# Performance work log

Measured on AMD Instinct MI355X. Metric: run time of the kernel, lower is better.

Reference implementation:

```python
import jax, jax.numpy as jnp
import numpy as np

N = 100_000   # nodes per type
E = 800_000   # edges per relation
H = 128       # hidden_channels
O = 64        # out_channels
TIME_SCALE = 1.0
LN_EPS = 1e-5


def setup_inputs() -> dict:
    key = jax.random.key(0)
    ks = jax.random.split(key, 24)
    nrm = lambda k, shp, s=1.0: jax.random.normal(k, shp, jnp.float32) * s
    inp = {}
    inp["x_A"] = nrm(ks[0], (N, H))
    inp["x_B"] = nrm(ks[1], (N, H))
    inp["x_C"] = nrm(ks[2], (N, H))
    inp["t_A"] = jax.random.uniform(ks[3], (N,), jnp.float32) * 1000.0
    inp["t_B"] = jax.random.uniform(ks[4], (N,), jnp.float32) * 1000.0
    inp["t_C"] = jax.random.uniform(ks[5], (N,), jnp.float32) * 1000.0
    inp["edge1"] = jnp.stack([jax.random.randint(ks[6], (E,), 0, N),
                              jax.random.randint(ks[7], (E,), 0, N)]).astype(jnp.int32)
    inp["edge2"] = jnp.stack([jax.random.randint(ks[8], (E,), 0, N),
                              jax.random.randint(ks[9], (E,), 0, N)]).astype(jnp.int32)
    kk = 10
    for i in range(2):
        inp[f"Wl{i}"] = nrm(ks[kk], (H, H), 0.05); kk += 1
        inp[f"bl{i}"] = jnp.zeros((H,), jnp.float32)
        inp[f"W0{i}"] = nrm(ks[kk], (H, H), 0.05); kk += 1
        inp[f"b0{i}"] = jnp.zeros((H,), jnp.float32)
        inp[f"W1{i}"] = nrm(ks[kk], (H, H), 0.05); kk += 1
        inp[f"b1{i}"] = jnp.zeros((H,), jnp.float32)
        inp[f"gate{i}"] = jnp.asarray(0.5, jnp.float32)
        inp[f"lam{i}"] = jnp.asarray(0.1, jnp.float32)  # raw lambda
        inp[f"lng{i}"] = jnp.ones((H,), jnp.float32)
        inp[f"lnb{i}"] = jnp.zeros((H,), jnp.float32)
    inp["Wout"] = nrm(ks[kk], (H, O), 0.05)
    inp["bout"] = jnp.zeros((O,), jnp.float32)
    return inp


def _layer(h_src, h_dst, x0_dst, edge, t_src, t_dst,
           Wl, bl, W0, b0, W1, b1, gate, raw_lam, lng, lnb):
    s, d = edge[0], edge[1]
    n_dst = h_dst.shape[0]
    # per-edge time-decay weight
    lam = jax.nn.softplus(raw_lam) + 1e-8
    delta = jnp.maximum((t_dst[d] - t_src[s]) / TIME_SCALE, 0.0)
    w = jnp.exp(jnp.maximum(-lam * delta, -60.0))          # [E]
    # gather + weight + scatter-add  (propagate with aggr='add')
    msg = h_src[s] * w[:, None]                            # [E,H]
    agg = jax.ops.segment_sum(msg, d, num_segments=n_dst)  # [n_dst,H]
    deg = jnp.maximum(jax.ops.segment_sum(w, d, num_segments=n_dst), 1e-6)
    out = agg / deg[:, None]
    g = jax.nn.sigmoid(gate)
    y = out @ Wl + bl + (1.0 - g) * (h_dst @ W0 + b0) + g * (x0_dst @ W1 + b1)
    y = jax.nn.relu(y)
    mu = jnp.mean(y, axis=-1, keepdims=True)
    var = jnp.mean((y - mu) ** 2, axis=-1, keepdims=True)
    y = (y - mu) * jax.lax.rsqrt(var + LN_EPS) * lng + lnb
    # index_copy_: only nodes that appear as a destination get updated
    cnt = jax.ops.segment_sum(jnp.ones_like(w), d, num_segments=n_dst)
    return jnp.where((cnt > 0)[:, None], y, h_dst)


def reference(x_A, x_B, x_C, t_A, t_B, t_C, edge1, edge2,
              Wl0, bl0, W00, b00, W10, b10, gate0, lam0, lng0, lnb0,
              Wl1, bl1, W01, b01, W11, b11, gate1, lam1, lng1, lnb1,
              Wout, bout):
    # reversed(metapath): process (B,r2,C) with conv_idx=1 first, then (A,r1,B) with conv_idx=0
    h_C = _layer(x_B, x_C, x_C, edge2, t_B, t_C,
                 Wl1, bl1, W01, b01, W11, b11, gate1, lam1, lng1, lnb1)
    h_B = _layer(x_A, x_B, x_B, edge1, t_A, t_B,
                 Wl0, bl0, W00, b00, W10, b10, gate0, lam0, lng0, lnb0)
    del h_B  # target type is metapath[-1][2] == 'C'; B's update does not feed C
    return h_C @ Wout + bout
```

## Files before the change

### kernel.cpp

```cpp
#include <hip/hip_runtime.h>


#define HD 128
#define OD 64
#define SCAN_E 1024

typedef unsigned short u16;
typedef short v8s __attribute__((ext_vector_type(8)));
typedef float v4f __attribute__((ext_vector_type(4)));

union Frag {
    unsigned int u[4];
    uint4 q;
    v8s v;
};

__device__ __forceinline__ float softplus_f(float x) {
    return fmaxf(x, 0.0f) + log1pf(expf(-fabsf(x)));
}
__device__ __forceinline__ float sigmoid_f(float x) {
    return 1.0f / (1.0f + expf(-x));
}
__device__ __forceinline__ int swz(int r, int c) {
    int g = (c >> 2) ^ (r & 7);
    return r * 128 + g * 4 + (c & 3);
}

__device__ __forceinline__ void split_store(float x, u16* ph, u16* pl) {
    unsigned int b = __float_as_uint(x);
    unsigned int h = b & 0xffff0000u;
    *ph = (u16)(h >> 16);
    float r = x - __uint_as_float(h);
    *pl = (u16)(__float_as_uint(r) >> 16);
}

__device__ __forceinline__ void cvt_split8(const float* f, unsigned int* hi,
                                           unsigned int* lo) {
#pragma unroll
    for (int j = 0; j < 4; ++j) {
        unsigned int b0 = __float_as_uint(f[2 * j]);
        unsigned int b1 = __float_as_uint(f[2 * j + 1]);
        unsigned int h0 = b0 & 0xffff0000u;
        unsigned int h1 = b1 & 0xffff0000u;
        hi[j] = (h0 >> 16) | h1;
        float r0 = f[2 * j]     - __uint_as_float(h0);
        float r1 = f[2 * j + 1] - __uint_as_float(h1);
        lo[j] = (__float_as_uint(r0) >> 16) | (__float_as_uint(r1) & 0xffff0000u);
    }
}

__global__ __launch_bounds__(256) void k_hist(
    const int* __restrict__ edge, int* __restrict__ cnt, int E)
{
    int e = blockIdx.x * 256 + threadIdx.x;
    if (e < E) atomicAdd(cnt + edge[E + e], 1);
}

__global__ __launch_bounds__(256) void k_scan1(
    const int* __restrict__ cnt, int* __restrict__ offs,
    int* __restrict__ part, int N)
{
    __shared__ int sh[256];
    const int t = threadIdx.x;
    const int base = blockIdx.x * SCAN_E + t * 4;
    int v[4], sum = 0;
#pragma unroll
    for (int i = 0; i < 4; ++i) {
        int idx = base + i;
        v[i] = (idx < N) ? cnt[idx] : 0;
        sum += v[i];
    }
    sh[t] = sum;
    __syncthreads();
    for (int off = 1; off < 256; off <<= 1) {
        int x = (t >= off) ? sh[t - off] : 0;
        __syncthreads();
        sh[t] += x;
        __syncthreads();
    }
    int run = (t > 0) ? sh[t - 1] : 0;
    if (t == 255) part[blockIdx.x] = sh[t];
#pragma unroll
    for (int i = 0; i < 4; ++i) {
        int idx = base + i;
        if (idx < N) offs[idx] = run;
        run += v[i];
    }
}

__global__ __launch_bounds__(128) void k_scan2(int* __restrict__ part, int NB)
{
    __shared__ int sh[128];
    const int t = threadIdx.x;
    sh[t] = (t < NB) ? part[t] : 0;
    __syncthreads();
    for (int off = 1; off < 128; off <<= 1) {
        int x = (t >= off) ? sh[t - off] : 0;
        __syncthreads();
        sh[t] += x;
        __syncthreads();
    }
    if (t < NB) part[t] = (t > 0) ? sh[t - 1] : 0;
}

__global__ __launch_bounds__(256) void k_fillw(
    const int* __restrict__ edge, const float* __restrict__ tB,
    const float* __restrict__ tC, const float* __restrict__ lam_raw,
    const int* __restrict__ offs, const int* __restrict__ part,
    int* __restrict__ fillc, int2* __restrict__ srcw, int E)
{
    int e = blockIdx.x * 256 + threadIdx.x;
    if (e >= E) return;
    int s = edge[e];
    int d = edge[E + e];
    float lam = softplus_f(lam_raw[0]) + 1e-8f;
    float dt  = fmaxf(tC[d] - tB[s], 0.0f);
    float w   = expf(fmaxf(-lam * dt, -60.0f));
    int pos = offs[d] + part[d >> 10] + atomicAdd(fillc + d, 1);
    srcw[pos] = make_int2(s, __float_as_int(w));
}

__global__ __launch_bounds__(256) void k_wprep(
    const float* __restrict__ Wl, const float* __restrict__ W0,
    const float* __restrict__ W1, const float* __restrict__ Wout,
    const float* __restrict__ bl, const float* __restrict__ b0,
    const float* __restrict__ b1, const float* __restrict__ gatep,
    u16* __restrict__ wlh, u16* __restrict__ wll,
    u16* __restrict__ wch, u16* __restrict__ wcl,
    u16* __restrict__ woh, u16* __restrict__ wol, float* __restrict__ bc)
{
    int i = blockIdx.x * 256 + threadIdx.x;
    const float g = sigmoid_f(gatep[0]);
    if (i < 16384) {
        int n = i >> 7, k = i & 127;
        float a  = Wl[k * 128 + n];
        float w0 = W0[k * 128 + n];
        float w1 = W1[k * 128 + n];
        float c  = (1.f - g) * w0 + g * w1;
        int off = ((k >> 5) * 128 + n) * 32 + (k & 31);
        split_store(a, wlh + off, wll + off);
        split_store(c, wch + off, wcl + off);
    } else if (i < 24576) {
        int j = i - 16384;
        int n = j >> 7, k = j & 127;
        float v = Wout[k * 64 + n];
        int off = ((k >> 5) * 64 + n) * 32 + (k & 31);
        split_store(v, woh + off, wol + off);
    } else if (i < 24704) {
        int t = i - 24576;
        bc[t] = bl[t] + (1.f - g) * b0[t] + g * b1[t];
    }
}

__global__ __launch_bounds__(256) void k_gather(
    const float* __restrict__ xB, const int2* __restrict__ srcw,
    const int* __restrict__ offs, const int* __restrict__ part,
    const int* __restrict__ cnt, float* __restrict__ aggn, int N)
{
    const int wave = (blockIdx.x * 256 + threadIdx.x) >> 6;
    const int lane = threadIdx.x & 63;
    const int slot = lane >> 4;
    const int l4   = lane & 15;
    if (wave >= N) return;
    const int r    = wave;
    const int degc = cnt[r];

    float* dstp = aggn + (size_t)r * HD;
    if (degc == 0) {
        if (slot == 0) {
            *reinterpret_cast<float4*>(dstp + l4 * 4) = make_float4(0, 0, 0, 0);
            *reinterpret_cast<float4*>(dstp + 64 + l4 * 4) = make_float4(0, 0, 0, 0);
        }
        return;
    }

    const int start = offs[r] + part[r >> 10];
    float4 a0 = make_float4(0, 0, 0, 0), a1 = make_float4(0, 0, 0, 0);
    float sw = 0.f;
#pragma unroll 2
    for (int j = slot; j < degc; j += 4) {
        int2 swp = srcw[start + j];
        float w = __int_as_float(swp.y);
        const float* row = xB + (size_t)swp.x * HD;
        float4 x0 = *reinterpret_cast<const float4*>(row + l4 * 4);
        float4 x1 = *reinterpret_cast<const float4*>(row + 64 + l4 * 4);
        a0.x = fmaf(w, x0.x, a0.x); a0.y = fmaf(w, x0.y, a0.y);
        a0.z = fmaf(w, x0.z, a0.z); a0.w = fmaf(w, x0.w, a0.w);
        a1.x = fmaf(w, x1.x, a1.x); a1.y = fmaf(w, x1.y, a1.y);
        a1.z = fmaf(w, x1.z, a1.z); a1.w = fmaf(w, x1.w, a1.w);
        sw += w;
    }
#pragma unroll
    for (int m = 16; m <= 32; m <<= 1) {
        a0.x += __shfl_xor(a0.x, m); a0.y += __shfl_xor(a0.y, m);
        a0.z += __shfl_xor(a0.z, m); a0.w += __shfl_xor(a0.w, m);
        a1.x += __shfl_xor(a1.x, m); a1.y += __shfl_xor(a1.y, m);
        a1.z += __shfl_xor(a1.z, m); a1.w += __shfl_xor(a1.w, m);
        sw   += __shfl_xor(sw, m);
    }
    float inv = 1.0f / fmaxf(sw, 1e-6f);
    if (slot == 0) {
        a0.x *= inv; a0.y *= inv; a0.z *= inv; a0.w *= inv;
        a1.x *= inv; a1.y *= inv; a1.z *= inv; a1.w *= inv;
        *reinterpret_cast<float4*>(dstp + l4 * 4) = a0;
        *reinterpret_cast<float4*>(dstp + 64 + l4 * 4) = a1;
    }
}

__global__ __launch_bounds__(256) void k_fused(
    const float* __restrict__ xC, const float* __restrict__ aggn,
    const int* __restrict__ cnt,
    const u16* __restrict__ wlh, const u16* __restrict__ wll,
    const u16* __restrict__ wch, const u16* __restrict__ wcl,
    const u16* __restrict__ woh, const u16* __restrict__ wol,
    const float* __restrict__ bc, const float* __restrict__ lng,
    const float* __restrict__ lnb, const float* __restrict__ bout,
    float* __restrict__ out, int N)
{
    __shared__ float lds[4 * 16 * 128];

    const int lane = threadIdx.x & 63;
    const int wid  = threadIdx.x >> 6;
    const int lr   = lane & 15;
    const int kb   = lane >> 4;
    const int row0 = blockIdx.x * 128 + wid * 32;
    float* myl = lds + wid * 16 * 128;

    v4f acc[2][8] = {};

#pragma unroll
    for (int mat = 0; mat < 2; ++mat) {
        const float* Asrc = mat ? xC : aggn;
        const uint4* BH = (const uint4*)(mat ? wch : wlh);
        const uint4* BL = (const uint4*)(mat ? wcl : wll);
#pragma unroll
        for (int kc = 0; kc < 4; ++kc) {
            Frag ah[2], al[2];
#pragma unroll
            for (int rt = 0; rt < 2; ++rt) {
                int r = row0 + rt * 16 + lr;
                r = (r < N) ? r : (N - 1);
                const float4* ap = (const float4*)(
                    Asrc + (size_t)r * HD + kc * 32 + kb * 8);
                float4 u0 = ap[0], u1 = ap[1];
                float f[8] = {u0.x, u0.y, u0.z, u0.w, u1.x, u1.y, u1.z, u1.w};
                cvt_split8(f, ah[rt].u, al[rt].u);
            }
#pragma unroll
            for (int ct = 0; ct < 8; ++ct) {
                int idx = kc * 512 + (ct * 16 + lr) * 4 + kb;
                Frag bh, bl;
                bh.q = BH[idx];
                bl.q = BL[idx];
#pragma unroll
                for (int rt = 0; rt < 2; ++rt) {
                    acc[rt][ct] = __builtin_amdgcn_mfma_f32_16x16x32_bf16(
                        ah[rt].v, bh.v, acc[rt][ct], 0, 0, 0);
                    acc[rt][ct] = __builtin_amdgcn_mfma_f32_16x16x32_bf16(
                        ah[rt].v, bl.v, acc[rt][ct], 0, 0, 0);
                    acc[rt][ct] = __builtin_amdgcn_mfma_f32_16x16x32_bf16(
                        al[rt].v, bh.v, acc[rt][ct], 0, 0, 0);
                }
            }
        }
    }

    float bcv[8], gav[8], bev[8];
#pragma unroll
    for (int ct = 0; ct < 8; ++ct) {
        int c = ct * 16 + lr;
        bcv[ct] = bc[c];
        gav[ct] = lng[c];
        bev[ct] = lnb[c];
    }
    float bov[4];
#pragma unroll
    for (int ct = 0; ct < 4; ++ct) bov[ct] = bout[ct * 16 + lr];

    const uint4* BH3 = (const uint4*)woh;
    const uint4* BL3 = (const uint4*)wol;

#pragma unroll
    for (int rt = 0; rt < 2; ++rt) {
        int rq = row0 + rt * 16 + kb * 4;
        int cvr[4] = {0, 0, 0, 0};
        if (rq < N) {
            int4 cv = *(const int4*)(cnt + rq);
            cvr[0] = cv.x; cvr[1] = cv.y; cvr[2] = cv.z; cvr[3] = cv.w;
        }
#pragma unroll
        for (int reg = 0; reg < 4; ++reg) {
            int rloc = kb * 4 + reg;
            int r    = rq + reg;
            float yv[8];
            float s = 0.f, q = 0.f;
#pragma unroll
            for (int ct = 0; ct < 8; ++ct) {
                float v = acc[rt][ct][reg] + bcv[ct];
                v = fmaxf(v, 0.0f);
                yv[ct] = v;
                s += v;
                q += v * v;
            }
#pragma unroll
            for (int m = 1; m < 16; m <<= 1) {
                s += __shfl_xor(s, m);
                q += __shfl_xor(q, m);
            }
            float mu   = s * (1.0f / 128.0f);
            float var  = q * (1.0f / 128.0f) - mu * mu;
            float rstd = rsqrtf(var + 1e-5f);

            if (r < N) {
                if (cvr[reg] > 0) {
#pragma unroll
                    for (int ct = 0; ct < 8; ++ct)
                        myl[swz(rloc, ct * 16 + lr)] =
                            (yv[ct] - mu) * rstd * gav[ct] + bev[ct];
                } else {
                    size_t base = (size_t)r * HD;
#pragma unroll
                    for (int ct = 0; ct < 8; ++ct)
                        myl[swz(rloc, ct * 16 + lr)] = xC[base + ct * 16 + lr];
                }
            } else {
#pragma unroll
                for (int ct = 0; ct < 8; ++ct)
                    myl[swz(rloc, ct * 16 + lr)] = 0.0f;
            }
        }

        v4f acc2[4] = {};
#pragma unroll
        for (int kc = 0; kc < 4; ++kc) {
            Frag ah, al;
            {
                int c0 = kc * 32 + kb * 8;
                float4 u0 = *reinterpret_cast<const float4*>(&myl[swz(lr, c0)]);
                float4 u1 = *reinterpret_cast<const float4*>(&myl[swz(lr, c0 + 4)]);
                float f[8] = {u0.x, u0.y, u0.z, u0.w, u1.x, u1.y, u1.z, u1.w};
                cvt_split8(f, ah.u, al.u);
            }
#pragma unroll
            for (int ct = 0; ct < 4; ++ct) {
                int idx = kc * 256 + (ct * 16 + lr) * 4 + kb;
                Frag bh, bl;
                bh.q = BH3[idx];
                bl.q = BL3[idx];
                acc2[ct] = __builtin_amdgcn_mfma_f32_16x16x32_bf16(
                    ah.v, bh.v, acc2[ct], 0, 0, 0);
                acc2[ct] = __builtin_amdgcn_mfma_f32_16x16x32_bf16(
                    ah.v, bl.v, acc2[ct], 0, 0, 0);
                acc2[ct] = __builtin_amdgcn_mfma_f32_16x16x32_bf16(
                    al.v, bh.v, acc2[ct], 0, 0, 0);
            }
        }

#pragma unroll
        for (int reg = 0; reg < 4; ++reg) {
            int r = rq + reg;
            if (r < N) {
#pragma unroll
                for (int ct = 0; ct < 4; ++ct)
                    out[(size_t)r * OD + ct * 16 + lr] = acc2[ct][reg] + bov[ct];
            }
        }
    }
}

extern "C" void kernel_launch(void* const* d_in, const int* in_sizes, int n_in,
                              void* d_out, int out_size, void* d_ws, size_t ws_size,
                              hipStream_t stream) {
    const float* xB    = (const float*)d_in[1];
    const float* xC    = (const float*)d_in[2];
    const float* tB    = (const float*)d_in[4];
    const float* tC    = (const float*)d_in[5];
    const int*   edge2 = (const int*)d_in[7];
    const float* Wl1   = (const float*)d_in[18];
    const float* bl1   = (const float*)d_in[19];
    const float* W01   = (const float*)d_in[20];
    const float* b01   = (const float*)d_in[21];
    const float* W11   = (const float*)d_in[22];
    const float* b11   = (const float*)d_in[23];
    const float* gate1 = (const float*)d_in[24];
    const float* lam1  = (const float*)d_in[25];
    const float* lng1  = (const float*)d_in[26];
    const float* lnb1  = (const float*)d_in[27];
    const float* Wout  = (const float*)d_in[28];
    const float* bout  = (const float*)d_in[29];

    const int N = in_sizes[2] / HD;
    const int E = in_sizes[7] / 2;

    int*   cnt   = (int*)d_ws;
    int*   fillc = cnt + N;
    int*   offs  = fillc + N;
    int*   part  = offs + N;
    int2*  srcw  = (int2*)(part + 128);
    u16*   wlh   = (u16*)(srcw + E);
    u16*   wll   = wlh + 16384;
    u16*   wch   = wll + 16384;
    u16*   wcl   = wch + 16384;
    u16*   woh   = wcl + 16384;
    u16*   wol   = woh + 8192;
    float* bc    = (float*)(wol + 8192);
    float* buf   = bc + 128;

    hipMemsetAsync(cnt, 0, (size_t)2 * N * sizeof(int), stream);

    dim3 blk(256);
    const int gE = (E + 255) / 256;
    const int NB = (N + SCAN_E - 1) / SCAN_E;

    k_wprep<<<97, blk, 0, stream>>>(Wl1, W01, W11, Wout, bl1, b01, b11, gate1,
                                    wlh, wll, wch, wcl, woh, wol, bc);
    k_hist <<<gE, blk, 0, stream>>>(edge2, cnt, E);
    k_scan1<<<NB, blk, 0, stream>>>(cnt, offs, part, N);
    k_scan2<<<1, 128, 0, stream>>>(part, NB);
    k_fillw<<<gE, blk, 0, stream>>>(edge2, tB, tC, lam1, offs, part, fillc, srcw, E);

    const int gN64 = (N * 64 + 255) / 256;
    k_gather<<<gN64, blk, 0, stream>>>(xB, srcw, offs, part, cnt, buf, N);

    const int GB = (N + 127) / 128;
    k_fused<<<GB, blk, 0, stream>>>(xC, buf, cnt, wlh, wll, wch, wcl, woh, wol,
                                    bc, lng1, lnb1, bout, (float*)d_out, N);
}
```

Baseline: 223.0 us.

## Fuse neighbor gather into the dense GEMM/LayerNorm kernel via LDS staging

Removes the separate gather kernel and its global intermediate buffer. Each wave now aggregates the weighted neighbor rows for its 16 destination rows straight into LDS, with half-waves taking alternate rows, and the first MFMA matmul reads its A operand from LDS. Rows per wave drop from 32 to 16 and blocks cover 64 rows, so the grid doubles. This saves a 51 MB write and read round trip plus one launch. The cost is a serial per-edge loop per half-wave, which gives less memory parallelism and more load imbalance than the old four-slot gather, and the weight fragments are reused across fewer rows.

```diff
diff --git a/kernel.cpp b/kernel.cpp
--- a/kernel.cpp
+++ b/kernel.cpp
@@ -152,64 +152,10 @@
     }
 }
 
-__global__ __launch_bounds__(256) void k_gather(
-    const float* __restrict__ xB, const int2* __restrict__ srcw,
-    const int* __restrict__ offs, const int* __restrict__ part,
-    const int* __restrict__ cnt, float* __restrict__ aggn, int N)
-{
-    const int wave = (blockIdx.x * 256 + threadIdx.x) >> 6;
-    const int lane = threadIdx.x & 63;
-    const int slot = lane >> 4;
-    const int l4   = lane & 15;
-    if (wave >= N) return;
-    const int r    = wave;
-    const int degc = cnt[r];
-
-    float* dstp = aggn + (size_t)r * HD;
-    if (degc == 0) {
-        if (slot == 0) {
-            *reinterpret_cast<float4*>(dstp + l4 * 4) = make_float4(0, 0, 0, 0);
-            *reinterpret_cast<float4*>(dstp + 64 + l4 * 4) = make_float4(0, 0, 0, 0);
-        }
-        return;
-    }
-
-    const int start = offs[r] + part[r >> 10];
-    float4 a0 = make_float4(0, 0, 0, 0), a1 = make_float4(0, 0, 0, 0);
-    float sw = 0.f;
-#pragma unroll 2
-    for (int j = slot; j < degc; j += 4) {
-        int2 swp = srcw[start + j];
-        float w = __int_as_float(swp.y);
-        const float* row = xB + (size_t)swp.x * HD;
-        float4 x0 = *reinterpret_cast<const float4*>(row + l4 * 4);
-        float4 x1 = *reinterpret_cast<const float4*>(row + 64 + l4 * 4);
-        a0.x = fmaf(w, x0.x, a0.x); a0.y = fmaf(w, x0.y, a0.y);
-        a0.z = fmaf(w, x0.z, a0.z); a0.w = fmaf(w, x0.w, a0.w);
-        a1.x = fmaf(w, x1.x, a1.x); a1.y = fmaf(w, x1.y, a1.y);
-        a1.z = fmaf(w, x1.z, a1.z); a1.w = fmaf(w, x1.w, a1.w);
-        sw += w;
-    }
-#pragma unroll
-    for (int m = 16; m <= 32; m <<= 1) {
-        a0.x += __shfl_xor(a0.x, m); a0.y += __shfl_xor(a0.y, m);
-        a0.z += __shfl_xor(a0.z, m); a0.w += __shfl_xor(a0.w, m);
-        a1.x += __shfl_xor(a1.x, m); a1.y += __shfl_xor(a1.y, m);
-        a1.z += __shfl_xor(a1.z, m); a1.w += __shfl_xor(a1.w, m);
-        sw   += __shfl_xor(sw, m);
-    }
-    float inv = 1.0f / fmaxf(sw, 1e-6f);
-    if (slot == 0) {
-        a0.x *= inv; a0.y *= inv; a0.z *= inv; a0.w *= inv;
-        a1.x *= inv; a1.y *= inv; a1.z *= inv; a1.w *= inv;
-        *reinterpret_cast<float4*>(dstp + l4 * 4) = a0;
-        *reinterpret_cast<float4*>(dstp + 64 + l4 * 4) = a1;
-    }
-}
-
 __global__ __launch_bounds__(256) void k_fused(
-    const float* __restrict__ xC, const float* __restrict__ aggn,
-    const int* __restrict__ cnt,
+    const float* __restrict__ xB, const float* __restrict__ xC,
+    const int* __restrict__ cnt, const int* __restrict__ offs,
+    const int* __restrict__ part, const int2* __restrict__ srcw,
     const u16* __restrict__ wlh, const u16* __restrict__ wll,
     const u16* __restrict__ wch, const u16* __restrict__ wcl,
     const u16* __restrict__ woh, const u16* __restrict__ wol,
@@ -223,28 +169,67 @@
     const int wid  = threadIdx.x >> 6;
     const int lr   = lane & 15;
     const int kb   = lane >> 4;
-    const int row0 = blockIdx.x * 128 + wid * 32;
+    const int row0 = blockIdx.x * 64 + wid * 16;
     float* myl = lds + wid * 16 * 128;
 
-    v4f acc[2][8] = {};
+    {
+        const int half = lane >> 5;
+        const int l32  = lane & 31;
+        for (int i = 0; i < 16; i += 2) {
+            int rloc = i + half;
+            int r    = row0 + rloc;
+            int deg = 0, start = 0;
+            if (r < N) {
+                deg   = cnt[r];
+                start = offs[r] + part[r >> 10];
+            }
+            float4 a = make_float4(0.f, 0.f, 0.f, 0.f);
+            float sumw = 0.f;
+#pragma unroll 2
+            for (int j = 0; j < deg; ++j) {
+                int2 sw = srcw[start + j];
+                float w = __int_as_float(sw.y);
+                const float4 x = *(reinterpret_cast<const float4*>(
+                                       xB + (size_t)sw.x * HD) + l32);
+                a.x = fmaf(w, x.x, a.x);
+                a.y = fmaf(w, x.y, a.y);
+                a.z = fmaf(w, x.z, a.z);
+                a.w = fmaf(w, x.w, a.w);
+                sumw += w;
+            }
+            float inv = 1.0f / fmaxf(sumw, 1e-6f);
+            *reinterpret_cast<float4*>(&myl[swz(rloc, l32 * 4)]) =
+                make_float4(a.x * inv, a.y * inv, a.z * inv, a.w * inv);
+        }
+    }
+
+    v4f acc[8] = {};
 
 #pragma unroll
     for (int mat = 0; mat < 2; ++mat) {
-        const float* Asrc = mat ? xC : aggn;
         const uint4* BH = (const uint4*)(mat ? wch : wlh);
         const uint4* BL = (const uint4*)(mat ? wcl : wll);
 #pragma unroll
         for (int kc = 0; kc < 4; ++kc) {
-            Frag ah[2], al[2];
-#pragma unroll
-            for (int rt = 0; rt < 2; ++rt) {
-                int r = row0 + rt * 16 + lr;
-                r = (r < N) ? r : (N - 1);
-                const float4* ap = (const float4*)(
-                    Asrc + (size_t)r * HD + kc * 32 + kb * 8);
-                float4 u0 = ap[0], u1 = ap[1];
-                float f[8] = {u0.x, u0.y, u0.z, u0.w, u1.x, u1.y, u1.z, u1.w};
-                cvt_split8(f, ah[rt].u, al[rt].u);
+            Frag ah, al;
+            {
+                float f[8];
+                if (mat == 0) {
+                    int c0 = kc * 32 + kb * 8;
+                    float4 u0 = *reinterpret_cast<const float4*>(&myl[swz(lr, c0)]);
+                    float4 u1 = *reinterpret_cast<const float4*>(&myl[swz(lr, c0 + 4)]);
+                    f[0] = u0.x; f[1] = u0.y; f[2] = u0.z; f[3] = u0.w;
+                    f[4] = u1.x; f[5] = u1.y; f[6] = u1.z; f[7] = u1.w;
+                } else {
+                    int r = row0 + lr;
+                    r = (r < N) ? r : (N - 1);
+                    const float4* ap = (const float4*)(
+                        xC + (size_t)r * HD + kc * 32 + kb * 8);
+                    float4 u0 = ap[0], u1 = ap[1];
+                    f[0] = u0.x; f[1] = u0.y; f[2] = u0.z; f[3] = u0.w;
+                    f[4] = u1.x; f[5] = u1.y; f[6] = u1.z; f[7] = u1.w;
+                }
+                cvt_split8(f, ah.u, al.u);
             }
 #pragma unroll
             for (int ct = 0; ct < 8; ++ct) {
@@ -252,15 +237,12 @@
                 Frag bh, bl;
                 bh.q = BH[idx];
                 bl.q = BL[idx];
-#pragma unroll
-                for (int rt = 0; rt < 2; ++rt) {
-                    acc[rt][ct] = __builtin_amdgcn_mfma_f32_16x16x32_bf16(
-                        ah[rt].v, bh.v, acc[rt][ct], 0, 0, 0);
-                    acc[rt][ct] = __builtin_amdgcn_mfma_f32_16x16x32_bf16(
-                        ah[rt].v, bl.v, acc[rt][ct], 0, 0, 0);
-                    acc[rt][ct] = __builtin_amdgcn_mfma_f32_16x16x32_bf16(
-                        al[rt].v, bh.v, acc[rt][ct], 0, 0, 0);
-                }
+                acc[ct] = __builtin_amdgcn_mfma_f32_16x16x32_bf16(
+                    ah.v, bh.v, acc[ct], 0, 0, 0);
+                acc[ct] = __builtin_amdgcn_mfma_f32_16x16x32_bf16(
+                    ah.v, bl.v, acc[ct], 0, 0, 0);
+                acc[ct] = __builtin_amdgcn_mfma_f32_16x16x32_bf16(
+                    al.v, bh.v, acc[ct], 0, 0, 0);
             }
         }
     }
@@ -273,16 +255,9 @@
         gav[ct] = lng[c];
         bev[ct] = lnb[c];
     }
-    float bov[4];
-#pragma unroll
-    for (int ct = 0; ct < 4; ++ct) bov[ct] = bout[ct * 16 + lr];
-
-    const uint4* BH3 = (const uint4*)woh;
-    const uint4* BL3 = (const uint4*)wol;
-
-#pragma unroll
-    for (int rt = 0; rt < 2; ++rt) {
-        int rq = row0 + rt * 16 + kb * 4;
+
+    {
+        int rq = row0 + kb * 4;
         int cvr[4] = {0, 0, 0, 0};
         if (rq < N) {
             int4 cv = *(const int4*)(cnt + rq);
@@ -296,7 +271,7 @@
             float s = 0.f, q = 0.f;
 #pragma unroll
             for (int ct = 0; ct < 8; ++ct) {
-                float v = acc[rt][ct][reg] + bcv[ct];
+                float v = acc[ct][reg] + bcv[ct];
                 v = fmaxf(v, 0.0f);
                 yv[ct] = v;
                 s += v;
@@ -329,41 +304,48 @@
                     myl[swz(rloc, ct * 16 + lr)] = 0.0f;
             }
         }
-
-        v4f acc2[4] = {};
-#pragma unroll
-        for (int kc = 0; kc < 4; ++kc) {
-            Frag ah, al;
-            {
-                int c0 = kc * 32 + kb * 8;
-                float4 u0 = *reinterpret_cast<const float4*>(&myl[swz(lr, c0)]);
-                float4 u1 = *reinterpret_cast<const float4*>(&myl[swz(lr, c0 + 4)]);
-                float f[8] = {u0.x, u0.y, u0.z, u0.w, u1.x, u1.y, u1.z, u1.w};
-                cvt_split8(f, ah.u, al.u);
-            }
-#pragma unroll
-            for (int ct = 0; ct < 4; ++ct) {
-                int idx = kc * 256 + (ct * 16 + lr) * 4 + kb;
-                Frag bh, bl;
-                bh.q = BH3[idx];
-                bl.q = BL3[idx];
-                acc2[ct] = __builtin_amdgcn_mfma_f32_16x16x32_bf16(
-                    ah.v, bh.v, acc2[ct], 0, 0, 0);
-                acc2[ct] = __builtin_amdgcn_mfma_f32_16x16x32_bf16(
-                    ah.v, bl.v, acc2[ct], 0, 0, 0);
-                acc2[ct] = __builtin_amdgcn_mfma_f32_16x16x32_bf16(
-                    al.v, bh.v, acc2[ct], 0, 0, 0);
-            }
-        }
-
-#pragma unroll
-        for (int reg = 0; reg < 4; ++reg) {
-            int r = rq + reg;
-            if (r < N) {
-#pragma unroll
-                for (int ct = 0; ct < 4; ++ct)
-                    out[(size_t)r * OD + ct * 16 + lr] = acc2[ct][reg] + bov[ct];
-            }
+    }
+
+    v4f acc2[4] = {};
+    const uint4* BH3 = (const uint4*)woh;
+    const uint4* BL3 = (const uint4*)wol;
+
+#pragma unroll
+    for (int kc = 0; kc < 4; ++kc) {
+        Frag ah, al;
+        {
+            int c0 = kc * 32 + kb * 8;
+            float4 u0 = *reinterpret_cast<const float4*>(&myl[swz(lr, c0)]);
+            float4 u1 = *reinterpret_cast<const float4*>(&myl[swz(lr, c0 + 4)]);
+            float f[8] = {u0.x, u0.y, u0.z, u0.w, u1.x, u1.y, u1.z, u1.w};
+            cvt_split8(f, ah.u, al.u);
+        }
+#pragma unroll
+        for (int ct = 0; ct < 4; ++ct) {
+            int idx = kc * 256 + (ct * 16 + lr) * 4 + kb;
+            Frag bh, bl;
+            bh.q = BH3[idx];
+            bl.q = BL3[idx];
+            acc2[ct] = __builtin_amdgcn_mfma_f32_16x16x32_bf16(
+                ah.v, bh.v, acc2[ct], 0, 0, 0);
+            acc2[ct] = __builtin_amdgcn_mfma_f32_16x16x32_bf16(
+                ah.v, bl.v, acc2[ct], 0, 0, 0);
+            acc2[ct] = __builtin_amdgcn_mfma_f32_16x16x32_bf16(
+                al.v, bh.v, acc2[ct], 0, 0, 0);
+        }
+    }
+
+    float bov[4];
+#pragma unroll
+    for (int ct = 0; ct < 4; ++ct) bov[ct] = bout[ct * 16 + lr];
+
+#pragma unroll
+    for (int reg = 0; reg < 4; ++reg) {
+        int r = row0 + kb * 4 + reg;
+        if (r < N) {
+#pragma unroll
+            for (int ct = 0; ct < 4; ++ct)
+                out[(size_t)r * OD + ct * 16 + lr] = acc2[ct][reg] + bov[ct];
         }
     }
 }
@@ -404,7 +386,6 @@
     u16*   woh   = wcl + 16384;
     u16*   wol   = woh + 8192;
     float* bc    = (float*)(wol + 8192);
-    float* buf   = bc + 128;
 
     hipMemsetAsync(cnt, 0, (size_t)2 * N * sizeof(int), stream);
 
@@ -419,10 +400,8 @@
     k_scan2<<<1, 128, 0, stream>>>(part, NB);
     k_fillw<<<gE, blk, 0, stream>>>(edge2, tB, tC, lam1, offs, part, fillc, srcw, E);
 
-    const int gN64 = (N * 64 + 255) / 256;
-    k_gather<<<gN64, blk, 0, stream>>>(xB, srcw, offs, part, cnt, buf, N);
-
-    const int GB = (N + 127) / 128;
-    k_fused<<<GB, blk, 0, stream>>>(xC, buf, cnt, wlh, wll, wch, wcl, woh, wol,
+    const int GB = (N + 63) / 64;
+    k_fused<<<GB, blk, 0, stream>>>(xB, xC, cnt, offs, part, srcw,
+                                    wlh, wll, wch, wcl, woh, wol,
                                     bc, lng1, lnb1, bout, (float*)d_out, N);
 }
```

New measurement: 251.5 us. +12.8%, slower.
